# Performance work log

Hardware: AMD Instinct MI355X
Metric: run time of the kernel (lower is better)

Reference implementation:

```python
import jax, jax.numpy as jnp
import numpy as np

B = 131072   # batch of (k0, k) evaluation points
N = 96       # number of layers in the multilayer stack


def setup_inputs() -> dict:
    key = jax.random.key(0)
    # Per-layer 4x4 propagation matrices for each batch point.
    # Keep them near-identity so the length-96 chain product stays numerically tame.
    noise = jax.random.normal(key, (B, N, 4, 4), dtype=jnp.float32)
    mats = jnp.eye(4, dtype=jnp.float32) + 0.05 * noise  # [B, N, 4, 4]
    return {"mats": mats}


def reference(mats):
    # ft.reduce(jnp.matmul, (L0, L1, ..., L_{N-1})) == ((L0 @ L1) @ L2) ... @ L_{N-1}
    # Left-to-right sequential chain product, vectorized over the batch via einsum.
    m0 = mats[:, 0]                                # [B, 4, 4]
    rest = jnp.moveaxis(mats[:, 1:], 1, 0)         # [N-1, B, 4, 4]

    def step(carry, m):
        return jnp.einsum('bij,bjk->bik', carry, m), None

    out, _ = jax.lax.scan(step, m0, rest)          # [B, 4, 4]
    return out
```

## Files before the change

### kernel.cpp

```cpp
#include <hip/hip_runtime.h>


template <int CTRL>
__device__ __forceinline__ float dpp_mov(float x) {
    int xi = __builtin_bit_cast(int, x);
    int r = __builtin_amdgcn_update_dpp(0, xi, CTRL, 0xF, 0xF, true);
    return __builtin_bit_cast(float, r);
}

template <int J>
__device__ __forceinline__ float4 quad_bcast(float4 m) {
    constexpr int C = J * 0x55;
    float4 r;
    r.x = dpp_mov<C>(m.x);
    r.y = dpp_mov<C>(m.y);
    r.z = dpp_mov<C>(m.z);
    r.w = dpp_mov<C>(m.w);
    return r;
}

__device__ __forceinline__ float4 row_times_mat(float4 v, float4 m) {
    float4 a = quad_bcast<0>(m);
    float4 acc;
    acc.x = v.x * a.x; acc.y = v.x * a.y; acc.z = v.x * a.z; acc.w = v.x * a.w;
    a = quad_bcast<1>(m);
    acc.x = fmaf(v.y, a.x, acc.x); acc.y = fmaf(v.y, a.y, acc.y);
    acc.z = fmaf(v.y, a.z, acc.z); acc.w = fmaf(v.y, a.w, acc.w);
    a = quad_bcast<2>(m);
    acc.x = fmaf(v.z, a.x, acc.x); acc.y = fmaf(v.z, a.y, acc.y);
    acc.z = fmaf(v.z, a.z, acc.z); acc.w = fmaf(v.z, a.w, acc.w);
    a = quad_bcast<3>(m);
    acc.x = fmaf(v.w, a.x, acc.x); acc.y = fmaf(v.w, a.y, acc.y);
    acc.z = fmaf(v.w, a.z, acc.z); acc.w = fmaf(v.w, a.w, acc.w);
    return acc;
}

__global__ __launch_bounds__(256, 8)
void chainmul_kernel(const float4* __restrict__ mats, float4* __restrict__ out) {
    const int t = blockIdx.x * 256 + threadIdx.x;
    const int b = t >> 2;
    const int r = t & 3;
    const float4* p = mats + (size_t)b * 384 + r;

    float4 v = p[0];
    float4 m = p[4];

#pragma unroll 4
    for (int n = 1; n < 95; ++n) {
        float4 mn = p[(size_t)4 * (n + 1)];
        v = row_times_mat(v, m);
        m = mn;
    }
    v = row_times_mat(v, m);

    out[(size_t)b * 4 + r] = v;
}

extern "C" void kernel_launch(void* const* d_in, const int* in_sizes, int n_in,
                              void* d_out, int out_size, void* d_ws, size_t ws_size,
                              hipStream_t stream) {
    const float4* mats = (const float4*)d_in[0];
    float4* out = (float4*)d_out;

    const int B = in_sizes[0] / (96 * 16);
    const int threads = B * 4;
    const int block = 256;
    const int grid = threads / block;

    hipLaunchKernelGGL(chainmul_kernel, dim3(grid), dim3(block), 0, stream,
                       mats, out);
}
```

Measured before the change: 152.2 us.

## Stage matrix chunks through LDS with async global_load_lds double buffering

Replaces the per-thread strided float4 loads with wave-cooperative global_load_lds transfers into a double-buffered LDS stage. Each wave loads contiguous 512-byte chunks of 8 matrices for 16 batch items, using an XOR swizzle to avoid bank conflicts, and prefetches the next chunk while it computes the current one. The chain now starts from the identity and multiplies in all 96 matrices. This aims to improve coalescing and overlap memory with compute, at the cost of 64KB of LDS per block, which limits occupancy.

```diff
diff --git a/kernel.cpp b/kernel.cpp
--- a/kernel.cpp
+++ b/kernel.cpp
@@ -1,5 +1,11 @@
 #include <hip/hip_runtime.h>
 
+
+typedef const void __attribute__((address_space(1))) gvoid_t;
+typedef void __attribute__((address_space(3))) lvoid_t;
+
+#define GLOAD_LDS16(g, l) \
+    __builtin_amdgcn_global_load_lds((gvoid_t*)(g), (lvoid_t*)(l), 16, 0, 0)
 
 template <int CTRL>
 __device__ __forceinline__ float dpp_mov(float x) {
@@ -35,25 +41,58 @@
     return acc;
 }
 
-__global__ __launch_bounds__(256, 8)
-void chainmul_kernel(const float4* __restrict__ mats, float4* __restrict__ out) {
-    const int t = blockIdx.x * 256 + threadIdx.x;
-    const int b = t >> 2;
-    const int r = t & 3;
-    const float4* p = mats + (size_t)b * 384 + r;
+__global__ __launch_bounds__(256)
+void chainmul_staged(const float4* __restrict__ mats, float4* __restrict__ out) {
+    __shared__ float4 stage[4096];
 
-    float4 v = p[0];
-    float4 m = p[4];
+    const int tid  = threadIdx.x;
+    const int wave = tid >> 6;
+    const int lane = tid & 63;
+    const int q    = lane >> 2;
+    const int r    = lane & 3;
+    const int wb0  = blockIdx.x * 64 + wave * 16;
 
-#pragma unroll 4
-    for (int n = 1; n < 95; ++n) {
-        float4 mn = p[(size_t)4 * (n + 1)];
-        v = row_times_mat(v, m);
-        m = mn;
+    const int hl = lane >> 5;
+    const int s  = lane & 31;
+
+    int src_base[8];
+#pragma unroll
+    for (int i = 0; i < 8; ++i) {
+        const int bl = 2 * i + hl;
+        src_base[i] = (wb0 + bl) * 384 + (s ^ (bl & 7));
     }
-    v = row_times_mat(v, m);
 
-    out[(size_t)b * 4 + r] = v;
+    float4* const wlds = &stage[wave * 1024];
+
+#pragma unroll
+    for (int i = 0; i < 8; ++i)
+        GLOAD_LDS16(mats + src_base[i], wlds + i * 64);
+
+    float4 v = make_float4(r == 0 ? 1.0f : 0.0f, r == 1 ? 1.0f : 0.0f,
+                           r == 2 ? 1.0f : 0.0f, r == 3 ? 1.0f : 0.0f);
+
+    for (int t = 0; t < 12; ++t) {
+        const int buf = t & 1;
+        if (t < 11) {
+            float4* const dst = wlds + (buf ^ 1) * 512;
+            const int off = (t + 1) * 32;
+#pragma unroll
+            for (int i = 0; i < 8; ++i)
+                GLOAD_LDS16(mats + src_base[i] + off, dst + i * 64);
+            asm volatile("s_waitcnt vmcnt(8)" ::: "memory");
+        } else {
+            asm volatile("s_waitcnt vmcnt(0)" ::: "memory");
+        }
+
+        const float4* const chunk = wlds + buf * 512 + q * 32;
+#pragma unroll
+        for (int m = 0; m < 8; ++m) {
+            const float4 row = chunk[(m * 4 + r) ^ (q & 7)];
+            v = row_times_mat(v, row);
+        }
+    }
+
+    out[(size_t)(wb0 + q) * 4 + r] = v;
 }
 
 extern "C" void kernel_launch(void* const* d_in, const int* in_sizes, int n_in,
@@ -63,10 +102,7 @@
     float4* out = (float4*)d_out;
 
     const int B = in_sizes[0] / (96 * 16);
-    const int threads = B * 4;
-    const int block = 256;
-    const int grid = threads / block;
-
-    hipLaunchKernelGGL(chainmul_kernel, dim3(grid), dim3(block), 0, stream,
+    const int grid = B / 64;
+    hipLaunchKernelGGL(chainmul_staged, dim3(grid), dim3(256), 0, stream,
                        mats, out);
 }
```

Result: faster. 147.9 us (-2.9%).

## Split each chain into 16 segments per wavefront and tree-reduce via shuffles

Applied to the files above, without the earlier changes.

The kernel now gives each batch's 96-matrix chain to a whole 64-lane wavefront instead of 4 lanes. The wavefront splits the chain into 16 segments of 6 matrices, computes the segment products in parallel, and combines them with a 4-level shuffle tree reduction. Each wavefront handles 4 batches in turn and double-buffers the matrix loads for the next batch. This shortens the serial dependency chain per thread and makes loads more coalesced, in exchange for extra shuffle traffic, more registers and a different floating-point summation order.

```diff
diff --git a/kernel.cpp b/kernel.cpp
--- a/kernel.cpp
+++ b/kernel.cpp
@@ -19,41 +19,83 @@
     return r;
 }
 
-__device__ __forceinline__ float4 row_times_mat(float4 v, float4 m) {
-    float4 a = quad_bcast<0>(m);
+__device__ __forceinline__ float4 rows_combine(float4 vl, float4 a0, float4 a1,
+                                               float4 a2, float4 a3) {
     float4 acc;
-    acc.x = v.x * a.x; acc.y = v.x * a.y; acc.z = v.x * a.z; acc.w = v.x * a.w;
-    a = quad_bcast<1>(m);
-    acc.x = fmaf(v.y, a.x, acc.x); acc.y = fmaf(v.y, a.y, acc.y);
-    acc.z = fmaf(v.y, a.z, acc.z); acc.w = fmaf(v.y, a.w, acc.w);
-    a = quad_bcast<2>(m);
-    acc.x = fmaf(v.z, a.x, acc.x); acc.y = fmaf(v.z, a.y, acc.y);
-    acc.z = fmaf(v.z, a.z, acc.z); acc.w = fmaf(v.z, a.w, acc.w);
-    a = quad_bcast<3>(m);
-    acc.x = fmaf(v.w, a.x, acc.x); acc.y = fmaf(v.w, a.y, acc.y);
-    acc.z = fmaf(v.w, a.z, acc.z); acc.w = fmaf(v.w, a.w, acc.w);
+    acc.x = vl.x * a0.x; acc.y = vl.x * a0.y; acc.z = vl.x * a0.z; acc.w = vl.x * a0.w;
+    acc.x = fmaf(vl.y, a1.x, acc.x); acc.y = fmaf(vl.y, a1.y, acc.y);
+    acc.z = fmaf(vl.y, a1.z, acc.z); acc.w = fmaf(vl.y, a1.w, acc.w);
+    acc.x = fmaf(vl.z, a2.x, acc.x); acc.y = fmaf(vl.z, a2.y, acc.y);
+    acc.z = fmaf(vl.z, a2.z, acc.z); acc.w = fmaf(vl.z, a2.w, acc.w);
+    acc.x = fmaf(vl.w, a3.x, acc.x); acc.y = fmaf(vl.w, a3.y, acc.y);
+    acc.z = fmaf(vl.w, a3.z, acc.z); acc.w = fmaf(vl.w, a3.w, acc.w);
     return acc;
 }
 
-__global__ __launch_bounds__(256, 8)
-void chainmul_kernel(const float4* __restrict__ mats, float4* __restrict__ out) {
-    const int t = blockIdx.x * 256 + threadIdx.x;
-    const int b = t >> 2;
-    const int r = t & 3;
-    const float4* p = mats + (size_t)b * 384 + r;
+__device__ __forceinline__ float4 row_times_mat(float4 v, float4 m) {
+    return rows_combine(v, quad_bcast<0>(m), quad_bcast<1>(m),
+                        quad_bcast<2>(m), quad_bcast<3>(m));
+}
 
-    float4 v = p[0];
-    float4 m = p[4];
+__device__ __forceinline__ float4 shfl4(float4 v, int src) {
+    float4 r;
+    r.x = __shfl(v.x, src);
+    r.y = __shfl(v.y, src);
+    r.z = __shfl(v.z, src);
+    r.w = __shfl(v.w, src);
+    return r;
+}
 
-#pragma unroll 4
-    for (int n = 1; n < 95; ++n) {
-        float4 mn = p[(size_t)4 * (n + 1)];
-        v = row_times_mat(v, m);
-        m = mn;
+__device__ __forceinline__ void load_mats(float4 dst[6], const float4* base) {
+#pragma unroll
+    for (int j = 0; j < 6; ++j) dst[j] = base[4 * j];
+}
+
+__device__ __forceinline__ float4 process(const float4 m[6], int q, int r) {
+    float4 v = m[0];
+#pragma unroll
+    for (int j = 1; j < 6; ++j) v = row_times_mat(v, m[j]);
+#pragma unroll
+    for (int L = 0; L < 4; ++L) {
+        const int lo = ((q & ~(1 << L)) << 2) + r;
+        const int hi = ((q | (1 << L)) << 2);
+        float4 vl = shfl4(v, lo);
+        float4 a0 = shfl4(v, hi + 0);
+        float4 a1 = shfl4(v, hi + 1);
+        float4 a2 = shfl4(v, hi + 2);
+        float4 a3 = shfl4(v, hi + 3);
+        v = rows_combine(vl, a0, a1, a2, a3);
     }
-    v = row_times_mat(v, m);
+    return v;
+}
 
-    out[(size_t)b * 4 + r] = v;
+__global__ __launch_bounds__(256)
+void chainmul_seg(const float4* __restrict__ mats, float4* __restrict__ out) {
+    const int lane = threadIdx.x & 63;
+    const int wg   = (blockIdx.x * 256 + threadIdx.x) >> 6;
+    const int q    = lane >> 2;
+    const int r    = lane & 3;
+    const int b0   = wg * 4;
+
+    const float4* base = mats + (size_t)b0 * 384 + q * 24 + r;
+
+    float4 mA[6], mB[6];
+    load_mats(mA, base);
+    load_mats(mB, base + 384);
+
+    float4 v = process(mA, q, r);
+    load_mats(mA, base + 768);
+    if (q == 0) out[(size_t)(b0 + 0) * 4 + r] = v;
+
+    v = process(mB, q, r);
+    load_mats(mB, base + 1152);
+    if (q == 0) out[(size_t)(b0 + 1) * 4 + r] = v;
+
+    v = process(mA, q, r);
+    if (q == 0) out[(size_t)(b0 + 2) * 4 + r] = v;
+
+    v = process(mB, q, r);
+    if (q == 0) out[(size_t)(b0 + 3) * 4 + r] = v;
 }
 
 extern "C" void kernel_launch(void* const* d_in, const int* in_sizes, int n_in,
@@ -63,10 +105,7 @@
     float4* out = (float4*)d_out;
 
     const int B = in_sizes[0] / (96 * 16);
-    const int threads = B * 4;
-    const int block = 256;
-    const int grid = threads / block;
-
-    hipLaunchKernelGGL(chainmul_kernel, dim3(grid), dim3(block), 0, stream,
+    const int grid = B / 16;
+    hipLaunchKernelGGL(chainmul_seg, dim3(grid), dim3(256), 0, stream,
                        mats, out);
 }
```

Measured after the change: 150.2 us. About the same (-1.4%).
